# Optimization experiments

Measured on AMD Instinct MI355X. Metric: run time of the kernel, lower is better.

The kernel has to match this reference:

```python
import jax, jax.numpy as jnp
import numpy as np
import math

D_MODEL = 1024
D_ATTN = 128
D_MID = 128
L = 4096

def setup_inputs() -> dict:
    key = jax.random.key(0)
    ks = jax.random.split(key, 5)
    scale = 1.0 / math.sqrt(D_MODEL)
    return {
        "x": jax.random.normal(ks[0], (L, D_MODEL), jnp.float32),
        "z": jax.random.normal(ks[1], (L, D_MODEL), jnp.float32),
        "Wq": jax.random.normal(ks[2], (D_MODEL, D_ATTN), jnp.float32) * scale,
        "bq": jnp.zeros((D_ATTN,), jnp.float32),
        "Wk": jax.random.normal(ks[3], (D_MODEL, D_ATTN), jnp.float32) * scale,
        "bk": jnp.zeros((D_ATTN,), jnp.float32),
        "Wv": jax.random.normal(ks[4], (D_MODEL, D_MID), jnp.float32) * scale,
        "bv": jnp.zeros((D_MID,), jnp.float32),
    }

def reference(x, z, Wq, bq, Wk, bk, Wv, bv):
    # q: [L_x, d_attn], k: [L_z, d_attn], v: [L_z, d_mid]
    q = x @ Wq + bq
    k = z @ Wk + bk
    v = z @ Wv + bv
    inv_sqrt_d = 1.0 / math.sqrt(D_ATTN)
    s = (q @ k.T) * inv_sqrt_d            # [L_x, L_z]
    y = jax.nn.softmax(s, axis=-1) @ v    # [L_x, d_mid]
    return y
```

## Files before the change

### kernel.cpp

```cpp
#include <hip/hip_runtime.h>
#include <hip/hip_bf16.h>

typedef __attribute__((ext_vector_type(8))) short short8;
typedef __attribute__((ext_vector_type(4))) float f32x4;

#define L_SEQ 4096
#define DM    1024
#define DA    128
#define AZ    16

#define OFF_QB  786432
#define OFF_KF  1835008
#define OFF_VF  2883584
#define OFF_OA  4063232

__device__ __forceinline__ short f2bf(float f) {
    union { float f; unsigned u; } v; v.f = f;
    unsigned u = v.u;
    u += 0x7FFFu + ((u >> 16) & 1u);
    return (short)(u >> 16);
}

__device__ __forceinline__ unsigned cvt_pk_bf16(float lo, float hi) {
    unsigned r;
    asm("v_cvt_pk_bf16_f32 %0, %1, %2" : "=v"(r) : "v"(lo), "v"(hi));
    return r;
}

typedef const __attribute__((address_space(1))) void g_void_t;
typedef __attribute__((address_space(3))) void l_void_t;
__device__ __forceinline__ void g2lds16(const void* g, void* l) {
    __builtin_amdgcn_global_load_lds((g_void_t*)g, (l_void_t*)l, 16, 0, 0);
}

__global__ __launch_bounds__(256) void prep_w_kernel(
    const float* __restrict__ Wq, const float* __restrict__ Wk,
    const float* __restrict__ Wv, short8* __restrict__ WTf)
{
    const int m = blockIdx.y, kidx = blockIdx.x;
    const float* __restrict__ W = (m == 0) ? Wq : (m == 1) ? Wk : Wv;
    __shared__ __align__(16) float Ws[32 * 132];
    const int t = threadIdx.x;
#pragma unroll
    for (int i = 0; i < 4; i++) {
        const int u = i * 256 + t;
        const int kk = u >> 5, n4 = (u & 31) * 4;
        *(f32x4*)&Ws[kk * 132 + n4] = *(const f32x4*)&W[(size_t)(kidx * 32 + kk) * DA + n4];
    }
    __syncthreads();
#pragma unroll
    for (int i = 0; i < 2; i++) {
        const int u = i * 256 + t;
        const int nt = u >> 6, lane = u & 63, l16 = lane & 15, quad = lane >> 4;
        short8 fr;
#pragma unroll
        for (int j = 0; j < 8; j++)
            fr[j] = f2bf(Ws[(quad * 8 + j) * 132 + nt * 16 + l16]);
        WTf[((size_t)(m * 32 + kidx) * 8 + nt) * 64 + lane] = fr;
    }
}

__global__ __launch_bounds__(256, 1) void qkv_kernel(
    const float* __restrict__ x, const float* __restrict__ z,
    const char* __restrict__ WTraw,
    const float* __restrict__ bq, const float* __restrict__ bk,
    const float* __restrict__ bv,
    short* __restrict__ qb, short8* __restrict__ kf, short8* __restrict__ vf)
{
    __shared__ __align__(16) char smem[2][32768];

    const int t = threadIdx.x;
    const int wave = t >> 6, lane = t & 63;
    const int l16 = lane & 15, quad = lane >> 4;
    const int mtile = wave >> 1, nhalf = wave & 1;
    const int isKV = blockIdx.y;
    const int m1 = isKV ? 1 : 0;
    const int row0 = blockIdx.x * 32;
    const int nbytes = isKV ? 32768 : 16384;

    const float* __restrict__ Am = isKV ? z : x;
    const float* ap = Am + (size_t)(row0 + mtile * 16 + l16) * DM + quad * 8;

    f32x4 acc1[4], acc2[4];
#pragma unroll
    for (int i = 0; i < 4; i++) {
        acc1[i] = (f32x4){0.f, 0.f, 0.f, 0.f};
        acc2[i] = (f32x4){0.f, 0.f, 0.f, 0.f};
    }

    auto stage = [&](int it2, int b) {
        const char* base1 = WTraw + (size_t)(m1 * 32 + it2 * 2) * 8192;
        const char* base2 = WTraw + (size_t)(2 * 32 + it2 * 2) * 8192;
#pragma unroll
        for (int i = 0; i < 8; i++) {
            const int off = i * 4096 + wave * 1024;
            if (off < nbytes) {
                const char* src = (off < 16384) ? (base1 + off) : (base2 + (off - 16384));
                g2lds16(src + lane * 16, &smem[b][off]);
            }
        }
    };

    f32x4 cur[4], nxt[4];
#pragma unroll
    for (int j = 0; j < 2; j++) {
        cur[j * 2]     = *(const f32x4*)(ap + j * 32);
        cur[j * 2 + 1] = *(const f32x4*)(ap + j * 32 + 4);
        nxt[j * 2]     = *(const f32x4*)(ap + 64 + j * 32);
        nxt[j * 2 + 1] = *(const f32x4*)(ap + 64 + j * 32 + 4);
    }

    stage(0, 0);
    __syncthreads();

#pragma unroll 1
    for (int it = 0; it < 16; it++) {
        const int b = it & 1;
        if (it + 1 < 16) stage(it + 1, b ^ 1);

        const int ipf = (it + 2 < 16) ? it + 2 : it;
        f32x4 fut[4];
#pragma unroll
        for (int j = 0; j < 2; j++) {
            fut[j * 2]     = *(const f32x4*)(ap + ipf * 64 + j * 32);
            fut[j * 2 + 1] = *(const f32x4*)(ap + ipf * 64 + j * 32 + 4);
        }

#pragma unroll
        for (int ss = 0; ss < 2; ss++) {
            short8 afr;
#pragma unroll
            for (int j = 0; j < 4; j++) {
                afr[j]     = f2bf(cur[ss * 2][j]);
                afr[4 + j] = f2bf(cur[ss * 2 + 1][j]);
            }
#pragma unroll
            for (int ntl = 0; ntl < 4; ntl++) {
                short8 bfr = *(const short8*)&smem[b][ss * 8192 + ((nhalf * 4 + ntl) * 64 + lane) * 16];
                acc1[ntl] = __builtin_amdgcn_mfma_f32_16x16x32_bf16(afr, bfr, acc1[ntl], 0, 0, 0);
            }
            if (isKV) {
#pragma unroll
                for (int ntl = 0; ntl < 4; ntl++) {
                    short8 bfr = *(const short8*)&smem[b][16384 + ss * 8192 + ((nhalf * 4 + ntl) * 64 + lane) * 16];
                    acc2[ntl] = __builtin_amdgcn_mfma_f32_16x16x32_bf16(afr, bfr, acc2[ntl], 0, 0, 0);
                }
            }
        }
        __syncthreads();
#pragma unroll
        for (int j = 0; j < 4; j++) { cur[j] = nxt[j]; nxt[j] = fut[j]; }
    }

    if (!isKV) {
        const float CL2E = 0.1275187669712930f;
#pragma unroll
        for (int ntl = 0; ntl < 4; ntl++) {
            const int col = nhalf * 64 + ntl * 16 + l16;
            const float bb = bq[col];
#pragma unroll
            for (int r = 0; r < 4; r++)
                qb[(size_t)(row0 + mtile * 16 + quad * 4 + r) * DA + col] =
                    f2bf((acc1[ntl][r] + bb) * CL2E);
        }
        return;
    }

    short* kT = (short*)&smem[0][0];
    short* vT = (short*)&smem[0][16384];
#pragma unroll
    for (int ntl = 0; ntl < 4; ntl++) {
        const int col = nhalf * 64 + ntl * 16 + l16;
        const float bbk = bk[col], bbv = bv[col];
#pragma unroll
        for (int r = 0; r < 4; r++) {
            const int rl = mtile * 16 + quad * 4 + r;
            kT[rl * 132 + col] = f2bf(acc1[ntl][r] + bbk);
            vT[rl * 132 + col] = f2bf(acc2[ntl][r] + bbv);
        }
    }
    __syncthreads();

    const int kg = blockIdx.x;
#pragma unroll
    for (int i = 0; i < 2; i++) {
        const int f = i * 256 + t;
        const int ks = f >> 7, nth = (f >> 6) & 1, ln = f & 63;
        const int lf = ln & 15, qf = ln >> 4;
        short8 fr;
#pragma unroll
        for (int j = 0; j < 8; j++)
            fr[j] = kT[(nth * 16 + lf) * 132 + ks * 32 + qf * 8 + j];
        kf[((size_t)(kg * 4 + ks) * 2 + nth) * 64 + ln] = fr;
    }
#pragma unroll
    for (int i = 0; i < 2; i++) {
        const int f = i * 256 + t;
        const int nt = f >> 6, ln = f & 63;
        const int lf = ln & 15, qf = ln >> 4;
        short8 fr;
#pragma unroll
        for (int j = 0; j < 8; j++)
            fr[j] = vT[(qf * 8 + j) * 132 + nt * 16 + lf];
        vf[((size_t)kg * 8 + nt) * 64 + ln] = fr;
    }
}

__global__ __launch_bounds__(256, 2) void attn_kernel(
    const short* __restrict__ qb, const char* __restrict__ kfg,
    const char* __restrict__ vfg, float* __restrict__ OA,
    float* __restrict__ lA)
{
    __shared__ __align__(16) char kv[2][16384];
    __shared__ __align__(16) short Ps[4][32 * 40];

    const int t    = threadIdx.x;
    const int wave = t >> 6;
    const int lane = t & 63;
    const int l16  = lane & 15;
    const int quad = lane >> 4;
    const int qr0  = blockIdx.x * 128;
    const int g0   = blockIdx.y * 8;

    auto stage = [&](int g, int b) {
        const char* kb_ = kfg + (size_t)(g0 + g) * 8192;
        const char* vb_ = vfg + (size_t)(g0 + g) * 8192;
#pragma unroll
        for (int i = 0; i < 4; i++) {
            const int off = i * 4096 + wave * 1024;
            const char* src = (off < 8192) ? (kb_ + off) : (vb_ + (off - 8192));
            g2lds16(src + lane * 16, &kv[b][off]);
        }
    };

    stage(0, 0);

    short8 af[2][4];
#pragma unroll
    for (int mt = 0; mt < 2; mt++) {
        const short* qrow = qb + (size_t)(qr0 + wave * 32 + mt * 16 + l16) * DA + quad * 8;
#pragma unroll
        for (int ks = 0; ks < 4; ks++)
            af[mt][ks] = *(const short8*)(qrow + ks * 32);
    }

    short8 bones;
#pragma unroll
    for (int j = 0; j < 8; j++) bones[j] = (l16 == 0) ? (short)0x3F80 : (short)0;

    f32x4 O[2][9];
#pragma unroll
    for (int mt = 0; mt < 2; mt++)
#pragma unroll
        for (int i = 0; i < 9; i++) O[mt][i] = (f32x4){0.f, 0.f, 0.f, 0.f};

    short* P = &Ps[wave][0];

    __syncthreads();

#pragma unroll 1
    for (int g = 0; g < 8; g++) {
        const int b = g & 1;
        if (g + 1 < 8) stage(g + 1, b ^ 1);

        const char* kb_ = &kv[b][0];
        const char* vb_ = &kv[b][8192];

        f32x4 s0[2][2];
#pragma unroll
        for (int mt = 0; mt < 2; mt++)
#pragma unroll
            for (int nh = 0; nh < 2; nh++) s0[mt][nh] = (f32x4){0.f, 0.f, 0.f, 0.f};
#pragma unroll
        for (int ks = 0; ks < 4; ks++)
#pragma unroll
            for (int nh = 0; nh < 2; nh++) {
                const short8 bfr = *(const short8*)(kb_ + ((ks * 2 + nh) * 64 + lane) * 16);
                s0[0][nh] = __builtin_amdgcn_mfma_f32_16x16x32_bf16(af[0][ks], bfr, s0[0][nh], 0, 0, 0);
                s0[1][nh] = __builtin_amdgcn_mfma_f32_16x16x32_bf16(af[1][ks], bfr, s0[1][nh], 0, 0, 0);
            }

        short8 b2v[8];
#pragma unroll
        for (int nt = 0; nt < 8; nt++)
            b2v[nt] = *(const short8*)(vb_ + (nt * 64 + lane) * 16);

#pragma unroll
        for (int mt = 0; mt < 2; mt++)
#pragma unroll
            for (int nh = 0; nh < 2; nh++)
#pragma unroll
                for (int rp = 0; rp < 2; rp++) {
                    const float e0 = exp2f(s0[mt][nh][rp * 2]);
                    const float e1 = exp2f(s0[mt][nh][rp * 2 + 1]);
                    const unsigned pk = cvt_pk_bf16(e0, e1);
                    const int row = mt * 16 + quad * 4 + rp * 2;
                    P[row * 40 + nh * 16 + l16]       = (short)(pk & 0xffff);
                    P[(row + 1) * 40 + nh * 16 + l16] = (short)(pk >> 16);
                }
        asm volatile("" ::: "memory");
        __builtin_amdgcn_s_waitcnt(0xc07f);
        asm volatile("" ::: "memory");

        short8 a2[2];
        a2[0] = *(const short8*)&P[l16 * 40 + quad * 8];
        a2[1] = *(const short8*)&P[(16 + l16) * 40 + quad * 8];
#pragma unroll
        for (int nt = 0; nt < 8; nt++) {
            O[0][nt] = __builtin_amdgcn_mfma_f32_16x16x32_bf16(a2[0], b2v[nt], O[0][nt], 0, 0, 0);
            O[1][nt] = __builtin_amdgcn_mfma_f32_16x16x32_bf16(a2[1], b2v[nt], O[1][nt], 0, 0, 0);
        }
        O[0][8] = __builtin_amdgcn_mfma_f32_16x16x32_bf16(a2[0], bones, O[0][8], 0, 0, 0);
        O[1][8] = __builtin_amdgcn_mfma_f32_16x16x32_bf16(a2[1], bones, O[1][8], 0, 0, 0);
        __syncthreads();
    }

    const int rw = qr0 + wave * 32;
    float* Ob = OA + (size_t)blockIdx.y * L_SEQ * DA;
#pragma unroll
    for (int mt = 0; mt < 2; mt++)
#pragma unroll
        for (int nt = 0; nt < 8; nt++)
#pragma unroll
            for (int r = 0; r < 4; r++)
                Ob[(size_t)(rw + mt * 16 + quad * 4 + r) * DA + nt * 16 + l16] = O[mt][nt][r];
    if (l16 == 0) {
        float* lb = lA + (size_t)blockIdx.y * L_SEQ;
#pragma unroll
        for (int mt = 0; mt < 2; mt++)
#pragma unroll
            for (int r = 0; r < 4; r++)
                lb[rw + mt * 16 + quad * 4 + r] = O[mt][8][r];
    }
}

__global__ __launch_bounds__(256) void merge_kernel(
    const float* __restrict__ OA, const float* __restrict__ lA,
    float* __restrict__ out)
{
    const int t = threadIdx.x;
    const int row = blockIdx.x * 16 + (t >> 4);
    const int cg = (t & 15) * 8;

    f32x4 a0 = (f32x4){0.f, 0.f, 0.f, 0.f};
    f32x4 a1 = (f32x4){0.f, 0.f, 0.f, 0.f};
    float lsum = 0.f;
#pragma unroll
    for (int zz = 0; zz < AZ; zz++) {
        const float* p = &OA[((size_t)zz * L_SEQ + row) * DA + cg];
        a0 = a0 + *(const f32x4*)p;
        a1 = a1 + *(const f32x4*)(p + 4);
        lsum += lA[(size_t)zz * L_SEQ + row];
    }
    const float inv = 1.f / lsum;
    f32x4* dst = (f32x4*)&out[(size_t)row * DA + cg];
    dst[0] = a0 * inv;
    dst[1] = a1 * inv;
}

extern "C" void kernel_launch(void* const* d_in, const int* in_sizes, int n_in,
                              void* d_out, int out_size, void* d_ws, size_t ws_size,
                              hipStream_t stream) {
    (void)in_sizes; (void)n_in; (void)out_size; (void)ws_size;
    const float* x  = (const float*)d_in[0];
    const float* z  = (const float*)d_in[1];
    const float* Wq = (const float*)d_in[2];
    const float* bq = (const float*)d_in[3];
    const float* Wk = (const float*)d_in[4];
    const float* bk = (const float*)d_in[5];
    const float* Wv = (const float*)d_in[6];
    const float* bv = (const float*)d_in[7];
    float* out = (float*)d_out;

    short8* WTf = (short8*)d_ws;
    short*  qb  = (short*)((char*)d_ws + OFF_QB);
    short8* kf  = (short8*)((char*)d_ws + OFF_KF);
    short8* vf  = (short8*)((char*)d_ws + OFF_VF);
    float*  OA  = (float*)((char*)d_ws + OFF_OA);
    float*  lA  = (float*)((char*)d_ws + OFF_OA + (size_t)AZ * L_SEQ * DA * 4);

    prep_w_kernel<<<dim3(32, 3), 256, 0, stream>>>(Wq, Wk, Wv, WTf);
    qkv_kernel<<<dim3(128, 2), 256, 0, stream>>>(x, z, (const char*)WTf,
                                                 bq, bk, bv, qb, kf, vf);
    attn_kernel<<<dim3(32, AZ), 256, 0, stream>>>(qb, (const char*)kf,
                                                  (const char*)vf, OA, lA);
    merge_kernel<<<256, 256, 0, stream>>>(OA, lA, out);
}
```

Before: 128.4 us.

## Software-pipeline PV MFMA one tile behind and store partials as fp16

The attention loop now double-buffers the per-wave P tile in LDS and carries the V fragments in registers, so the P·V MFMAs for the previous key group run after the current group's exp and P writes. This removes the explicit LDS waitcnt stall between writing P and reading it back. Separately, the split-K partial outputs are written as fp16 instead of fp32, halving the OA traffic between the attention and merge kernels. The cost is extra VGPRs for the carried V fragments, more LDS for the second P buffer, and reduced precision in the unnormalized partial sums, which could risk overflow or rounding error.

```diff
diff --git a/kernel.cpp b/kernel.cpp
--- a/kernel.cpp
+++ b/kernel.cpp
@@ -3,6 +3,7 @@
 
 typedef __attribute__((ext_vector_type(8))) short short8;
 typedef __attribute__((ext_vector_type(4))) float f32x4;
+typedef __attribute__((ext_vector_type(8))) _Float16 half8;
 
 #define L_SEQ 4096
 #define DM    1024
@@ -13,6 +14,7 @@
 #define OFF_KF  1835008
 #define OFF_VF  2883584
 #define OFF_OA  4063232
+#define OA_BYTES ((size_t)AZ * L_SEQ * DA * 2)
 
 __device__ __forceinline__ short f2bf(float f) {
     union { float f; unsigned u; } v; v.f = f;
@@ -208,11 +210,11 @@
 
 __global__ __launch_bounds__(256, 2) void attn_kernel(
     const short* __restrict__ qb, const char* __restrict__ kfg,
-    const char* __restrict__ vfg, float* __restrict__ OA,
+    const char* __restrict__ vfg, _Float16* __restrict__ OA,
     float* __restrict__ lA)
 {
     __shared__ __align__(16) char kv[2][16384];
-    __shared__ __align__(16) short Ps[4][32 * 40];
+    __shared__ __align__(16) short Ps[4][2][32 * 40];
 
     const int t    = threadIdx.x;
     const int wave = t >> 6;
@@ -254,7 +256,7 @@
 #pragma unroll
         for (int i = 0; i < 9; i++) O[mt][i] = (f32x4){0.f, 0.f, 0.f, 0.f};
 
-    short* P = &Ps[wave][0];
+    short8 bvC[8];
 
     __syncthreads();
 
@@ -280,11 +282,19 @@
                 s0[1][nh] = __builtin_amdgcn_mfma_f32_16x16x32_bf16(af[1][ks], bfr, s0[1][nh], 0, 0, 0);
             }
 
-        short8 b2v[8];
+        short8 bvN[8];
 #pragma unroll
         for (int nt = 0; nt < 8; nt++)
-            b2v[nt] = *(const short8*)(vb_ + (nt * 64 + lane) * 16);
-
+            bvN[nt] = *(const short8*)(vb_ + (nt * 64 + lane) * 16);
+
+        short8 a2[2];
+        if (g > 0) {
+            const short* Pp = &Ps[wave][b ^ 1][0];
+            a2[0] = *(const short8*)&Pp[l16 * 40 + quad * 8];
+            a2[1] = *(const short8*)&Pp[(16 + l16) * 40 + quad * 8];
+        }
+
+        short* P = &Ps[wave][b][0];
 #pragma unroll
         for (int mt = 0; mt < 2; mt++)
 #pragma unroll
@@ -298,32 +308,47 @@
                     P[row * 40 + nh * 16 + l16]       = (short)(pk & 0xffff);
                     P[(row + 1) * 40 + nh * 16 + l16] = (short)(pk >> 16);
                 }
-        asm volatile("" ::: "memory");
-        __builtin_amdgcn_s_waitcnt(0xc07f);
-        asm volatile("" ::: "memory");
-
+
+        if (g > 0) {
+#pragma unroll
+            for (int nt = 0; nt < 8; nt++) {
+                O[0][nt] = __builtin_amdgcn_mfma_f32_16x16x32_bf16(a2[0], bvC[nt], O[0][nt], 0, 0, 0);
+                O[1][nt] = __builtin_amdgcn_mfma_f32_16x16x32_bf16(a2[1], bvC[nt], O[1][nt], 0, 0, 0);
+            }
+            O[0][8] = __builtin_amdgcn_mfma_f32_16x16x32_bf16(a2[0], bones, O[0][8], 0, 0, 0);
+            O[1][8] = __builtin_amdgcn_mfma_f32_16x16x32_bf16(a2[1], bones, O[1][8], 0, 0, 0);
+        }
+
+#pragma unroll
+        for (int nt = 0; nt < 8; nt++) bvC[nt] = bvN[nt];
+
+        __syncthreads();
+    }
+
+    {
+        const short* Pp = &Ps[wave][1][0];
         short8 a2[2];
-        a2[0] = *(const short8*)&P[l16 * 40 + quad * 8];
-        a2[1] = *(const short8*)&P[(16 + l16) * 40 + quad * 8];
+        a2[0] = *(const short8*)&Pp[l16 * 40 + quad * 8];
+        a2[1] = *(const short8*)&Pp[(16 + l16) * 40 + quad * 8];
 #pragma unroll
         for (int nt = 0; nt < 8; nt++) {
-            O[0][nt] = __builtin_amdgcn_mfma_f32_16x16x32_bf16(a2[0], b2v[nt], O[0][nt], 0, 0, 0);
-            O[1][nt] = __builtin_amdgcn_mfma_f32_16x16x32_bf16(a2[1], b2v[nt], O[1][nt], 0, 0, 0);
+            O[0][nt] = __builtin_amdgcn_mfma_f32_16x16x32_bf16(a2[0], bvC[nt], O[0][nt], 0, 0, 0);
+            O[1][nt] = __builtin_amdgcn_mfma_f32_16x16x32_bf16(a2[1], bvC[nt], O[1][nt], 0, 0, 0);
         }
         O[0][8] = __builtin_amdgcn_mfma_f32_16x16x32_bf16(a2[0], bones, O[0][8], 0, 0, 0);
         O[1][8] = __builtin_amdgcn_mfma_f32_16x16x32_bf16(a2[1], bones, O[1][8], 0, 0, 0);
-        __syncthreads();
     }
 
     const int rw = qr0 + wave * 32;
-    float* Ob = OA + (size_t)blockIdx.y * L_SEQ * DA;
+    _Float16* Ob = OA + (size_t)blockIdx.y * L_SEQ * DA;
 #pragma unroll
     for (int mt = 0; mt < 2; mt++)
 #pragma unroll
         for (int nt = 0; nt < 8; nt++)
 #pragma unroll
             for (int r = 0; r < 4; r++)
-                Ob[(size_t)(rw + mt * 16 + quad * 4 + r) * DA + nt * 16 + l16] = O[mt][nt][r];
+                Ob[(size_t)(rw + mt * 16 + quad * 4 + r) * DA + nt * 16 + l16] =
+                    (_Float16)O[mt][nt][r];
     if (l16 == 0) {
         float* lb = lA + (size_t)blockIdx.y * L_SEQ;
 #pragma unroll
@@ -335,27 +360,31 @@
 }
 
 __global__ __launch_bounds__(256) void merge_kernel(
-    const float* __restrict__ OA, const float* __restrict__ lA,
+    const _Float16* __restrict__ OA, const float* __restrict__ lA,
     float* __restrict__ out)
 {
     const int t = threadIdx.x;
     const int row = blockIdx.x * 16 + (t >> 4);
     const int cg = (t & 15) * 8;
 
-    f32x4 a0 = (f32x4){0.f, 0.f, 0.f, 0.f};
-    f32x4 a1 = (f32x4){0.f, 0.f, 0.f, 0.f};
+    float acc[8];
+#pragma unroll
+    for (int j = 0; j < 8; j++) acc[j] = 0.f;
     float lsum = 0.f;
 #pragma unroll
     for (int zz = 0; zz < AZ; zz++) {
-        const float* p = &OA[((size_t)zz * L_SEQ + row) * DA + cg];
-        a0 = a0 + *(const f32x4*)p;
-        a1 = a1 + *(const f32x4*)(p + 4);
+        const half8 v = *(const half8*)&OA[((size_t)zz * L_SEQ + row) * DA + cg];
+#pragma unroll
+        for (int j = 0; j < 8; j++) acc[j] += (float)v[j];
         lsum += lA[(size_t)zz * L_SEQ + row];
     }
     const float inv = 1.f / lsum;
+    f32x4 o0, o1;
+#pragma unroll
+    for (int j = 0; j < 4; j++) { o0[j] = acc[j] * inv; o1[j] = acc[4 + j] * inv; }
     f32x4* dst = (f32x4*)&out[(size_t)row * DA + cg];
-    dst[0] = a0 * inv;
-    dst[1] = a1 * inv;
+    dst[0] = o0;
+    dst[1] = o1;
 }
 
 extern "C" void kernel_launch(void* const* d_in, const int* in_sizes, int n_in,
@@ -372,12 +401,12 @@
     const float* bv = (const float*)d_in[7];
     float* out = (float*)d_out;
 
-    short8* WTf = (short8*)d_ws;
-    short*  qb  = (short*)((char*)d_ws + OFF_QB);
-    short8* kf  = (short8*)((char*)d_ws + OFF_KF);
-    short8* vf  = (short8*)((char*)d_ws + OFF_VF);
-    float*  OA  = (float*)((char*)d_ws + OFF_OA);
-    float*  lA  = (float*)((char*)d_ws + OFF_OA + (size_t)AZ * L_SEQ * DA * 4);
+    short8*   WTf = (short8*)d_ws;
+    short*    qb  = (short*)((char*)d_ws + OFF_QB);
+    short8*   kf  = (short8*)((char*)d_ws + OFF_KF);
+    short8*   vf  = (short8*)((char*)d_ws + OFF_VF);
+    _Float16* OA  = (_Float16*)((char*)d_ws + OFF_OA);
+    float*    lA  = (float*)((char*)d_ws + OFF_OA + OA_BYTES);
 
     prep_w_kernel<<<dim3(32, 3), 256, 0, stream>>>(Wq, Wk, Wv, WTf);
     qkv_kernel<<<dim3(128, 2), 256, 0, stream>>>(x, z, (const char*)WTf,
```

Result: no change. 127.9 us (-0.4%).
